# Performance work log

Measured on AMD Instinct MI355X. Metric: run time of the kernel, lower is better.

## Reference

```python
import jax, jax.numpy as jnp
import numpy as np

INFLUENCE_RADIUS = 8  # VectorizedTrajectoryComputer default


def compute_trajectories(emb):
    # emb: [B, S, D] -> [B, S, D]
    B, S, D = emb.shape
    diffs = emb[:, 1:] - emb[:, :-1]                      # [B, S-1, D]
    mag = jnp.linalg.norm(diffs, axis=-1, keepdims=True)  # [B, S-1, 1]
    ntraj = diffs / jnp.maximum(mag, 1e-8)                # normalized trajectories
    mw = jnp.tanh(mag[..., 0])                            # magnitude weights [B, S-1]
    pos = jnp.arange(S)[:, None]                          # [S, 1]
    j = jnp.arange(S - 1)[None, :]                        # [1, S-1]
    ws = jnp.maximum(0, pos - INFLUENCE_RADIUS)           # window start per pos
    mask = (j >= ws) & (j < pos)                          # window_end = pos (pos <= S-1)
    wsz = jnp.maximum(pos - ws, 1)                        # window size (>=1 to avoid /0)
    recency = jnp.where(mask, (j - ws + 1) / wsz, 0.0).astype(emb.dtype)  # [S, S-1]
    cw = mw[:, None, :] * recency[None]                   # combined weights [B, S, S-1]
    nw = cw / jnp.maximum(cw.sum(-1, keepdims=True), 1e-8)
    return jnp.einsum('bpj,bjd->bpd', nw, ntraj)          # [B, S, D]


def setup_inputs() -> dict:
    key = jax.random.key(0)
    ks = jax.random.split(key, 6)
    B, S, D = 2, 2048, 1024
    H, K, hd = 16, 16, 64
    return {
        'x': jax.random.normal(ks[0], (B, S, D), dtype=jnp.float32),
        'qkv_w': jax.random.normal(ks[1], (3 * D, D), dtype=jnp.float32) * 0.02,
        'out_w': jax.random.normal(ks[2], (D, D), dtype=jnp.float32) * 0.02,
        'splat_centers': jax.random.normal(ks[3], (H, K, hd), dtype=jnp.float32) * 0.02,
        'splat_log_scales': jnp.zeros((H, K), dtype=jnp.float32),
        'splat_amplitudes': jnp.ones((H, K), dtype=jnp.float32),
    }


def reference(x, qkv_w, out_w, splat_centers, splat_log_scales, splat_amplitudes):
    B, S, D = x.shape
    H, K, hd = splat_centers.shape
    # trajectories (computed when trajectories=None in forward)
    traj = compute_trajectories(x)
    # qkv projection (no bias)
    qkv = x @ qkv_w.T                                      # [B, S, 3D]
    q, k, v = jnp.split(qkv, 3, axis=-1)
    def heads(t):
        return t.reshape(B, S, H, hd).transpose(0, 2, 1, 3)  # [B, H, S, hd]
    q, k, v = heads(q), heads(k), heads(v)
    # squared distances to splat centers: [B, H, S, K]
    cn = jnp.sum(splat_centers ** 2, axis=-1)              # [H, K]
    def dists_sq(t):
        tn = jnp.sum(t ** 2, axis=-1, keepdims=True)       # [B, H, S, 1]
        cross = jnp.einsum('bhsd,hkd->bhsk', t, splat_centers)
        return tn - 2.0 * cross + cn[None, :, None, :]
    scales_sq = jnp.exp(splat_log_scales)[None, :, None, :] ** 2  # [1, H, 1, K]
    amp = jax.nn.sigmoid(splat_amplitudes)[None, :, None, :]
    q_weights = jnp.exp(-0.5 * dists_sq(q) / scales_sq) * amp     # [B, H, S, K]
    k_weights = jnp.exp(-0.5 * dists_sq(k) / scales_sq) * amp
    attn = jnp.einsum('bhis,bhjs->bhij', q_weights, k_weights)    # [B, H, S, S]
    attn = jax.nn.softmax(attn, axis=-1)
    out = jnp.einsum('bhij,bhjd->bhid', attn, v)                  # [B, H, S, hd]
    out = out.transpose(0, 2, 1, 3).reshape(B, S, D) @ out_w.T    # [B, S, D]
    return out, traj
```

## Files before the change

### kernel.cpp

```cpp
#include <hip/hip_runtime.h>
#include <math.h>

#define SEQ 2048
#define DIM 1024
#define NB  2
#define NH  16

typedef __attribute__((ext_vector_type(8))) short short8;
typedef __attribute__((ext_vector_type(4))) float floatx4;
typedef __attribute__((ext_vector_type(16))) float floatx16;

__device__ __forceinline__ ushort f2bf(float f) {
    unsigned u = __float_as_uint(f);
    return (ushort)((u + 0x7FFFu + ((u >> 16) & 1u)) >> 16);
}
__device__ __forceinline__ float bf2f(ushort h) {
    return __uint_as_float(((unsigned)h) << 16);
}
__device__ __forceinline__ void gload16(const void* g, char* lds_base) {
    __builtin_amdgcn_global_load_lds(
        (const __attribute__((address_space(1))) void*)g,
        (__attribute__((address_space(3))) void*)lds_base, 16, 0, 0);
}
__device__ __forceinline__ unsigned cvtpk(float a, float b) {
    unsigned r;
    asm("v_cvt_pk_bf16_f32 %0, %1, %2" : "=v"(r) : "v"(a), "v"(b));
    return r;
}
__device__ __forceinline__ void plswap(unsigned &a, unsigned &b) {
    asm("v_permlane32_swap_b32 %0, %1" : "+v"(a), "+v"(b));
}

__global__ __launch_bounds__(256) void cvt_split_kernel(
    const float* __restrict__ src, ushort* __restrict__ hi, ushort* __restrict__ lo, int n)
{
    int i = (blockIdx.x * 256 + threadIdx.x) * 4;
    if (i >= n) return;
    float4 v = *(const float4*)(src + i);
    ushort4 h, l;
    h.x = f2bf(v.x); l.x = f2bf(v.x - bf2f(h.x));
    h.y = f2bf(v.y); l.y = f2bf(v.y - bf2f(h.y));
    h.z = f2bf(v.z); l.z = f2bf(v.z - bf2f(h.z));
    h.w = f2bf(v.w); l.w = f2bf(v.w - bf2f(h.w));
    *(ushort4*)(hi + i) = h;
    *(ushort4*)(lo + i) = l;
}

__global__ __launch_bounds__(256) void cvt_front_kernel(
    const float* __restrict__ x, const float* __restrict__ qkv_w,
    ushort* __restrict__ xh, ushort* __restrict__ xl,
    ushort* __restrict__ wh, ushort* __restrict__ wlv)
{
    const int blk = blockIdx.x;
    if (blk < 4096) {
        int i = blk * 1024 + threadIdx.x * 4;
        float4 v = *(const float4*)(x + i);
        ushort4 h, l;
        h.x = f2bf(v.x); l.x = f2bf(v.x - bf2f(h.x));
        h.y = f2bf(v.y); l.y = f2bf(v.y - bf2f(h.y));
        h.z = f2bf(v.z); l.z = f2bf(v.z - bf2f(h.z));
        h.w = f2bf(v.w); l.w = f2bf(v.w - bf2f(h.w));
        *(ushort4*)(xh + i) = h;
        *(ushort4*)(xl + i) = l;
    } else if (blk < 6144) {
        int i = (blk - 4096) * 1024 + threadIdx.x * 4;
        float4 v = *(const float4*)(qkv_w + i);
        ushort4 o;
        o.x = f2bf(v.x); o.y = f2bf(v.y); o.z = f2bf(v.z); o.w = f2bf(v.w);
        *(ushort4*)(wh + i) = o;
    } else {
        int i = (blk - 6144) * 1024 + threadIdx.x * 4;
        float4 v = *(const float4*)(qkv_w + 2097152 + i);
        ushort4 h, l;
        h.x = f2bf(v.x); l.x = f2bf(v.x - bf2f(h.x));
        h.y = f2bf(v.y); l.y = f2bf(v.y - bf2f(h.y));
        h.z = f2bf(v.z); l.z = f2bf(v.z - bf2f(h.z));
        h.w = f2bf(v.w); l.w = f2bf(v.w - bf2f(h.w));
        *(ushort4*)(wh + 2097152 + i) = h;
        *(ushort4*)(wlv + i) = l;
    }
}

__global__ __launch_bounds__(256) void traj_stats_kernel(
    const float* __restrict__ x, float* __restrict__ sbuf, float* __restrict__ invbuf)
{
    const int wave = threadIdx.x >> 6;
    const int lane = threadIdx.x & 63;
    const int row  = blockIdx.x * 4 + wave;
    const int NR = NB * (SEQ - 1);
    if (row >= NR) return;
    const int b = row / (SEQ - 1);
    const int j = row - b * (SEQ - 1);
    const float* x0 = x + ((size_t)(b * SEQ + j)) * DIM;
    const float* x1 = x0 + DIM;
    float sum = 0.f;
    #pragma unroll
    for (int q = 0; q < 4; ++q) {
        int idx = q * 256 + lane * 4;
        float4 a = *(const float4*)(x0 + idx);
        float4 c = *(const float4*)(x1 + idx);
        float dx = c.x-a.x, dy = c.y-a.y, dz = c.z-a.z, dw = c.w-a.w;
        sum += dx*dx + dy*dy + dz*dz + dw*dw;
    }
    #pragma unroll
    for (int off = 32; off > 0; off >>= 1) sum += __shfl_down(sum, off);
    if (lane == 0) {
        float mag = sqrtf(sum);
        sbuf[row]   = tanhf(mag);
        invbuf[row] = 1.0f / fmaxf(mag, 1e-8f);
    }
}

__global__ __launch_bounds__(256) void traj_kernel(
    const float* __restrict__ x, const float* __restrict__ sbuf,
    const float* __restrict__ invbuf, float* __restrict__ traj_out)
{
    const int bp = blockIdx.x;
    const int b  = bp >> 11;
    const int p  = bp & (SEQ - 1);
    int ws = p - 8; if (ws < 0) ws = 0;
    const int wlen = p - ws;
    const float wsz = (float)((p - ws) > 1 ? (p - ws) : 1);
    const int base = b * (SEQ - 1) + ws;

    float Z = 0.f;
    for (int t = 0; t < wlen; ++t)
        Z += sbuf[base + t] * ((float)(t + 1) / wsz);
    const float scale = 1.0f / fmaxf(Z, 1e-8f);

    const int d0 = threadIdx.x * 4;
    const float* xb = x + ((size_t)(b * SEQ + ws)) * DIM + d0;
    float4 prev = *(const float4*)xb;
    float4 acc = make_float4(0.f,0.f,0.f,0.f);
    for (int t = 0; t < wlen; ++t) {
        xb += DIM;
        float4 cur = *(const float4*)xb;
        float cc = sbuf[base + t] * ((float)(t + 1) / wsz) * invbuf[base + t] * scale;
        acc.x += cc * (cur.x - prev.x);
        acc.y += cc * (cur.y - prev.y);
        acc.z += cc * (cur.z - prev.z);
        acc.w += cc * (cur.w - prev.w);
        prev = cur;
    }
    *(float4*)(traj_out + (size_t)bp * DIM + d0) = acc;
}

template<int SPLIT, int EPI, int BN>
__global__ __launch_bounds__(256) void mfma_gemm(
    const ushort* __restrict__ Ah, const ushort* __restrict__ Al,
    const ushort* __restrict__ Bh, const ushort* __restrict__ Bl,
    float* __restrict__ cout, int ldc,
    ushort* __restrict__ qwb, ushort* __restrict__ kwb)
{
    constexpr int JT   = BN / 32;
    constexpr int BSZ  = BN * 64;
    constexpr int HALF = 8192 + BSZ;
    constexpr int SMEM = (SPLIT ? 2 : 1) * HALF;
    __shared__ __align__(16) char smem[SMEM];
    const int tid = threadIdx.x;
    const int l = tid & 63;
    const int w = tid >> 6;
    const int wm = w >> 1, wn = w & 1;
    const int n0 = blockIdx.x * BN;
    const int m0 = blockIdx.y * 128;

    char* a_h = smem;
    char* b_h = smem + 8192;
    char* a_l = smem + HALF;
    char* b_l = smem + HALF + 8192;

    const int srowA = 32 * w + (l >> 2);
    const int srowB = (BN == 128 ? 32 * w : 16 * w) + (l >> 2);
    const int scol  = (l & 3) * 8;
    const ushort* Ahg = Ah + (size_t)(m0 + srowA) * 1024 + scol;
    const ushort* Bhg = Bh + (size_t)(n0 + srowB) * 1024 + scol;
    const ushort* Alg = SPLIT ? Al + (size_t)(m0 + srowA) * 1024 + scol : nullptr;
    const ushort* Blg = SPLIT ? Bl + (size_t)(n0 + srowB) * 1024 + scol : nullptr;

    floatx4 acc[4][JT] = {};
    const int fr = l & 15;
    const int fq = (l >> 4) * 16;

    for (int kb = 0; kb < 1024; kb += 32) {
        if (kb) __syncthreads();
        gload16(Ahg + kb,             a_h + w*2048);
        gload16(Ahg + kb + 16*1024,   a_h + w*2048 + 1024);
        if (BN == 128) {
            gload16(Bhg + kb,             b_h + w*2048);
            gload16(Bhg + kb + 16*1024,   b_h + w*2048 + 1024);
        } else {
            gload16(Bhg + kb,             b_h + w*1024);
        }
        if (SPLIT) {
            gload16(Alg + kb,           a_l + w*2048);
            gload16(Alg + kb + 16*1024, a_l + w*2048 + 1024);
            if (BN == 128) {
                gload16(Blg + kb,           b_l + w*2048);
                gload16(Blg + kb + 16*1024, b_l + w*2048 + 1024);
            } else {
                gload16(Blg + kb,           b_l + w*1024);
            }
        }
        __syncthreads();
        short8 fah[4], fbh[JT], fal[4], fbl[JT];
        #pragma unroll
        for (int t = 0; t < 4; ++t) {
            fah[t] = *(const short8*)(a_h + ((wm*64 + t*16 + fr) << 6) + fq);
            if (SPLIT)
                fal[t] = *(const short8*)(a_l + ((wm*64 + t*16 + fr) << 6) + fq);
        }
        #pragma unroll
        for (int t = 0; t < JT; ++t) {
            fbh[t] = *(const short8*)(b_h + ((wn*(BN/2) + t*16 + fr) << 6) + fq);
            if (SPLIT)
                fbl[t] = *(const short8*)(b_l + ((wn*(BN/2) + t*16 + fr) << 6) + fq);
        }
        #pragma unroll
        for (int it = 0; it < 4; ++it)
            #pragma unroll
            for (int jt = 0; jt < JT; ++jt) {
                acc[it][jt] = __builtin_amdgcn_mfma_f32_16x16x32_bf16(
                    fah[it], fbh[jt], acc[it][jt], 0, 0, 0);
                if (SPLIT) {
                    acc[it][jt] = __builtin_amdgcn_mfma_f32_16x16x32_bf16(
                        fah[it], fbl[jt], acc[it][jt], 0, 0, 0);
                    acc[it][jt] = __builtin_amdgcn_mfma_f32_16x16x32_bf16(
                        fal[it], fbh[jt], acc[it][jt], 0, 0, 0);
                }
            }
    }

    const int row0 = (l >> 4) * 4;
    const int col  = l & 15;

    if (EPI == 0) {
        #pragma unroll
        for (int it = 0; it < 4; ++it)
            #pragma unroll
            for (int jt = 0; jt < JT; ++jt)
                #pragma unroll
                for (int r = 0; r < 4; ++r) {
                    int gm = m0 + wm*64 + it*16 + row0 + r;
                    int gn = n0 + wn*(BN/2) + jt*16 + col;
                    cout[(size_t)gm * ldc + gn] = acc[it][jt][r];
                }
    } else if (EPI == 2) {
        #pragma unroll
        for (int it = 0; it < 4; ++it)
            #pragma unroll
            for (int jt = 0; jt < JT; ++jt)
                #pragma unroll
                for (int r = 0; r < 4; ++r) {
                    int md = m0 + wm*64 + it*16 + row0 + r;
                    int t  = n0 + wn*(BN/2) + jt*16 + col;
                    int bb = t >> 11, ss = t & (SEQ - 1);
                    qwb[((size_t)bb << 21) + (size_t)md * SEQ + ss] = f2bf(acc[it][jt][r]);
                }
    } else {
        ushort* obuf = (n0 < 1024) ? qwb : kwb;
        const int nb = n0 & 1023;
        #pragma unroll
        for (int it = 0; it < 4; ++it)
            #pragma unroll
            for (int jt = 0; jt < JT; ++jt)
                #pragma unroll
                for (int r = 0; r < 4; ++r) {
                    int gm = m0 + wm*64 + it*16 + row0 + r;
                    int gn = nb + wn*(BN/2) + jt*16 + col;
                    int hh = gn >> 6, d = gn & 63;
                    int bb = gm >> 11, ss = gm & (SEQ - 1);
                    obuf[(((size_t)(bb*NH + hh))*SEQ + ss)*64 + d] = f2bf(acc[it][jt][r]);
                }
    }
}

__global__ __launch_bounds__(256) void splat_kernel(
    const ushort* __restrict__ qin, const ushort* __restrict__ kin,
    ushort* __restrict__ wq, ushort* __restrict__ wk,
    const float* __restrict__ centers, const float* __restrict__ lscales,
    const float* __restrict__ amps)
{
    __shared__ float Cs[16*64];
    __shared__ float Pr[48];
    const int tid = threadIdx.x;
    const int isK = blockIdx.x >> 8;
    const int bx  = blockIdx.x & 255;
    const ushort* qk = isK ? kin : qin;
    ushort* wout = isK ? wk : wq;
    const int bh  = bx >> 3;
    const int h   = bh & 15;
    const int s   = (bx & 7) * 256 + tid;
    {
        float4 c4 = *(const float4*)(centers + (size_t)h*1024 + tid*4);
        *(float4*)(Cs + tid*4) = c4;
    }
    if (tid < 16) {
        float s2 = __expf(2.f * lscales[h*16 + tid]);
        Pr[tid]      = -0.5f / s2;
        Pr[16 + tid] = 1.f / (1.f + __expf(-amps[h*16 + tid]));
        const float* cp = centers + ((size_t)h*16 + tid)*64;
        float cn = 0.f;
        for (int i = 0; i < 64; ++i) cn += cp[i]*cp[i];
        Pr[32 + tid] = cn;
    }
    __syncthreads();

    float q[64];
    const ushort* qp = qk + ((size_t)bh*SEQ + s)*64;
    #pragma unroll
    for (int i = 0; i < 8; ++i) {
        short8 v = *(const short8*)(qp + i*8);
        #pragma unroll
        for (int j = 0; j < 8; ++j) q[i*8+j] = bf2f((ushort)v[j]);
    }
    float tn = 0.f;
    #pragma unroll
    for (int i = 0; i < 64; ++i) tn = fmaf(q[i], q[i], tn);

    ushort o16[16];
    #pragma unroll 4
    for (int sp = 0; sp < 16; ++sp) {
        const float* cp = Cs + sp*64;
        float cr = 0.f;
        #pragma unroll
        for (int i = 0; i < 64; ++i) cr = fmaf(q[i], cp[i], cr);
        float dq = tn - 2.f*cr + Pr[32 + sp];
        o16[sp] = f2bf(__expf(dq * Pr[sp]) * Pr[16 + sp]);
    }
    ushort* op = wout + ((size_t)bh*SEQ + s)*16;
    *(short8*)(op)     = *(short8*)(o16);
    *(short8*)(op + 8) = *(short8*)(o16 + 8);
}

__global__ __launch_bounds__(256, 4) void attn_kernel(
    const ushort* __restrict__ qw, const ushort* __restrict__ kw,
    const ushort* __restrict__ vbt, ushort* __restrict__ hoh, ushort* __restrict__ hol)
{
    __shared__ __align__(16) char smem[16384 + 512];
    const int tid = threadIdx.x;
    const int l   = tid & 63;
    const int w   = tid >> 6;
    const int qh  = w >> 1;
    const int kh  = w & 1;
    const int l31 = l & 31;
    const int hi  = l >> 5;
    const int bh = blockIdx.y;
    const int b = bh >> 4;
    const int h = bh & 15;
    const int s0 = blockIdx.x * 64;

    short8 qf = *(const short8*)(qw + ((size_t)bh*SEQ + s0 + qh*32 + l31)*16 + hi*8);

    const ushort* kfp = kw + ((size_t)bh*SEQ + kh*32 + l31)*16 + hi*8;
    const ushort* vtb = vbt + ((size_t)(b*1024 + h*64))*SEQ;

    const int dA = w*16 + (l >> 3);
    const int dB = dA + 8;
    const ushort* vsA = vtb + (size_t)dA*SEQ + ((l & 7) ^ (dA & 7))*8;
    const ushort* vsB = vtb + (size_t)dB*SEQ + ((l & 7) ^ (dB & 7))*8;

    floatx16 acc0 = {}, acc1 = {};
    floatx16 zero16 = {};
    float zpart = 0.f;

    gload16(vsA, smem + w*2048);
    gload16(vsB, smem + w*2048 + 1024);
    short8 kf = *(const short8*)kfp;

    for (int jt = 0; jt < 32; ++jt) {
        __syncthreads();
        char* bufn = smem + ((jt + 1) & 1)*8192;
        if (jt < 31) {
            gload16(vsA + (jt + 1)*64, bufn + w*2048);
            gload16(vsB + (jt + 1)*64, bufn + w*2048 + 1024);
        }
        floatx16 sc = __builtin_amdgcn_mfma_f32_32x32x16_bf16(kf, qf, zero16, 0, 0, 0);
        if (jt < 31) kf = *(const short8*)(kfp + (jt + 1)*1024);

        float e[16];
        #pragma unroll
        for (int r = 0; r < 16; ++r) e[r] = __expf(sc[r]);
        float zs = 0.f;
        #pragma unroll
        for (int r = 0; r < 16; ++r) zs += e[r];
        zpart += zs;

        unsigned p0 = cvtpk(e[0],  e[1]),  p1 = cvtpk(e[2],  e[3]);
        unsigned p2 = cvtpk(e[4],  e[5]),  p3 = cvtpk(e[6],  e[7]);
        unsigned p4 = cvtpk(e[8],  e[9]),  p5 = cvtpk(e[10], e[11]);
        unsigned p6 = cvtpk(e[12], e[13]), p7 = cvtpk(e[14], e[15]);
        plswap(p0, p2); plswap(p1, p3);
        plswap(p4, p6); plswap(p5, p7);
        union { unsigned u[4]; short8 s; } ua, ub;
        ua.u[0] = p0; ua.u[1] = p1; ua.u[2] = p2; ua.u[3] = p3;
        ub.u[0] = p4; ub.u[1] = p5; ub.u[2] = p6; ub.u[3] = p7;

        const ushort* buf = (const ushort*)(smem + (jt & 1)*8192);
        #pragma unroll
        for (int dt = 0; dt < 2; ++dt) {
            int row = dt*32 + l31;
            const ushort* vr = buf + row*64;
            int bk0 = (kh*4 + hi)     ^ (row & 7);
            int bk1 = (kh*4 + 2 + hi) ^ (row & 7);
            short8 vb0 = *(const short8*)(vr + bk0*8);
            short8 vb1 = *(const short8*)(vr + bk1*8);
            if (dt == 0) {
                acc0 = __builtin_amdgcn_mfma_f32_32x32x16_bf16(ua.s, vb0, acc0, 0, 0, 0);
                acc0 = __builtin_amdgcn_mfma_f32_32x32x16_bf16(ub.s, vb1, acc0, 0, 0, 0);
            } else {
                acc1 = __builtin_amdgcn_mfma_f32_32x32x16_bf16(ua.s, vb0, acc1, 0, 0, 0);
                acc1 = __builtin_amdgcn_mfma_f32_32x32x16_bf16(ub.s, vb1, acc1, 0, 0, 0);
            }
        }
    }

    __syncthreads();

    float* cb = (float*)smem;
    float* zb = (float*)(smem + 16384);

    unsigned za = __float_as_uint(zpart), zc = za;
    plswap(za, zc);
    float zq = __uint_as_float(za) + __uint_as_float(zc);
    if (l31 == l) zb[kh*64 + qh*32 + l31] = zq;

    if (kh) {
        #pragma unroll
        for (int r = 0; r < 16; ++r) {
            int q = (r & 3) + 8*(r >> 2) + 4*hi;
            cb[(qh*32 + q)*64 + l31]      = acc0[r];
            cb[(qh*32 + q)*64 + 32 + l31] = acc1[r];
        }
    }
    __syncthreads();
    if (!kh) {
        #pragma unroll
        for (int r = 0; r < 16; ++r) {
            int q = (r & 3) + 8*(r >> 2) + 4*hi;
            float zt = zb[qh*32 + q] + zb[64 + qh*32 + q];
            float inv = 1.0f / zt;
            int s = s0 + qh*32 + q;
            size_t base = ((size_t)(b*SEQ + s))*1024 + h*64;
            float v0 = (acc0[r] + cb[(qh*32 + q)*64 + l31])      * inv;
            float v1 = (acc1[r] + cb[(qh*32 + q)*64 + 32 + l31]) * inv;
            ushort h0 = f2bf(v0);
            ushort h1 = f2bf(v1);
            hoh[base + l31]      = h0;
            hol[base + l31]      = f2bf(v0 - bf2f(h0));
            hoh[base + 32 + l31] = h1;
            hol[base + 32 + l31] = f2bf(v1 - bf2f(h1));
        }
    }
}

extern "C" void kernel_launch(void* const* d_in, const int* in_sizes, int n_in,
                              void* d_out, int out_size, void* d_ws, size_t ws_size,
                              hipStream_t stream)
{
    const float* x       = (const float*)d_in[0];
    const float* qkv_w   = (const float*)d_in[1];
    const float* out_w   = (const float*)d_in[2];
    const float* centers = (const float*)d_in[3];
    const float* lscales = (const float*)d_in[4];
    const float* amps    = (const float*)d_in[5];
    float* out  = (float*)d_out;
    float* traj = out + (size_t)NB*SEQ*DIM;

    char* wsb = (char*)d_ws;
    ushort* xh   = (ushort*)(wsb);
    ushort* xl   = (ushort*)(wsb + (8u<<20));
    ushort* wh   = (ushort*)(wsb + (16u<<20));
    ushort* wlv  = (ushort*)(wsb + (22u<<20));
    ushort* vbt  = (ushort*)(wsb + (24u<<20));
    float*  sbuf = (float*)(wsb + (40u<<20));
    float*  invb = sbuf + 4096;
    ushort* qbuf = xl;
    ushort* kbuf = (ushort*)(wsb + (32u<<20));
    ushort* qwbh = wlv;
    ushort* kwbh = wh + 2048*1024;
    ushort* owh  = wh;
    ushort* owl  = wh + 1048576;
    ushort* hoh  = xh;
    ushort* hol  = xl;

    cvt_front_kernel<<<7168, 256, 0, stream>>>(x, qkv_w, xh, xl, wh, wlv);
    traj_stats_kernel<<<1024, 256, 0, stream>>>(x, sbuf, invb);
    traj_kernel<<<NB*SEQ, 256, 0, stream>>>(x, sbuf, invb, traj);
    mfma_gemm<1,2,64><<<dim3(64, 8), 256, 0, stream>>>(
        wh + 2048*1024, wlv, xh, xl, nullptr, 0, vbt, nullptr);
    mfma_gemm<0,3,128><<<dim3(16, 32), 256, 0, stream>>>(
        xh, nullptr, wh, nullptr, nullptr, 0, qbuf, kbuf);
    splat_kernel<<<512, 256, 0, stream>>>(qbuf, kbuf, qwbh, kwbh, centers, lscales, amps);
    cvt_split_kernel<<<1024, 256, 0, stream>>>(out_w, owh, owl, 1048576);
    attn_kernel<<<dim3(32, 32), 256, 0, stream>>>(qwbh, kwbh, vbt, hoh, hol);
    mfma_gemm<1,0,64><<<dim3(16, 32), 256, 0, stream>>>(
        hoh, hol, owh, owl, out, 1024, nullptr, nullptr);
}
```

Measured before the change: 270.5 us.

## Merge independent small kernels into combined launches to cut kernel count

Folds the trajectory-stats pass into the front conversion kernel and the out_w conversion into the splat kernel. It also splits the trajectory kernel across the V and QK GEMM launches via block-index dispatch, taking the launch count from nine to six. The aim is to remove launch overhead and the tail bubbles between small kernels by letting independent work fill idle CUs. In exchange, the GEMM launches carry the larger LDS footprint on the trajectory blocks too, which could lower occupancy for those blocks.

```diff
diff --git a/kernel.cpp b/kernel.cpp
--- a/kernel.cpp
+++ b/kernel.cpp
@@ -31,25 +31,11 @@
     asm("v_permlane32_swap_b32 %0, %1" : "+v"(a), "+v"(b));
 }
 
-__global__ __launch_bounds__(256) void cvt_split_kernel(
-    const float* __restrict__ src, ushort* __restrict__ hi, ushort* __restrict__ lo, int n)
-{
-    int i = (blockIdx.x * 256 + threadIdx.x) * 4;
-    if (i >= n) return;
-    float4 v = *(const float4*)(src + i);
-    ushort4 h, l;
-    h.x = f2bf(v.x); l.x = f2bf(v.x - bf2f(h.x));
-    h.y = f2bf(v.y); l.y = f2bf(v.y - bf2f(h.y));
-    h.z = f2bf(v.z); l.z = f2bf(v.z - bf2f(h.z));
-    h.w = f2bf(v.w); l.w = f2bf(v.w - bf2f(h.w));
-    *(ushort4*)(hi + i) = h;
-    *(ushort4*)(lo + i) = l;
-}
-
-__global__ __launch_bounds__(256) void cvt_front_kernel(
+__global__ __launch_bounds__(256) void front_kernel(
     const float* __restrict__ x, const float* __restrict__ qkv_w,
     ushort* __restrict__ xh, ushort* __restrict__ xl,
-    ushort* __restrict__ wh, ushort* __restrict__ wlv)
+    ushort* __restrict__ wh, ushort* __restrict__ wlv,
+    float* __restrict__ sbuf, float* __restrict__ invbuf)
 {
     const int blk = blockIdx.x;
     if (blk < 4096) {
@@ -68,7 +54,7 @@
         ushort4 o;
         o.x = f2bf(v.x); o.y = f2bf(v.y); o.z = f2bf(v.z); o.w = f2bf(v.w);
         *(ushort4*)(wh + i) = o;
-    } else {
+    } else if (blk < 7168) {
         int i = (blk - 6144) * 1024 + threadIdx.x * 4;
         float4 v = *(const float4*)(qkv_w + 2097152 + i);
         ushort4 h, l;
@@ -78,44 +64,39 @@
         h.w = f2bf(v.w); l.w = f2bf(v.w - bf2f(h.w));
         *(ushort4*)(wh + 2097152 + i) = h;
         *(ushort4*)(wlv + i) = l;
-    }
-}
-
-__global__ __launch_bounds__(256) void traj_stats_kernel(
-    const float* __restrict__ x, float* __restrict__ sbuf, float* __restrict__ invbuf)
-{
-    const int wave = threadIdx.x >> 6;
-    const int lane = threadIdx.x & 63;
-    const int row  = blockIdx.x * 4 + wave;
-    const int NR = NB * (SEQ - 1);
-    if (row >= NR) return;
-    const int b = row / (SEQ - 1);
-    const int j = row - b * (SEQ - 1);
-    const float* x0 = x + ((size_t)(b * SEQ + j)) * DIM;
-    const float* x1 = x0 + DIM;
-    float sum = 0.f;
-    #pragma unroll
-    for (int q = 0; q < 4; ++q) {
-        int idx = q * 256 + lane * 4;
-        float4 a = *(const float4*)(x0 + idx);
-        float4 c = *(const float4*)(x1 + idx);
-        float dx = c.x-a.x, dy = c.y-a.y, dz = c.z-a.z, dw = c.w-a.w;
-        sum += dx*dx + dy*dy + dz*dz + dw*dw;
-    }
-    #pragma unroll
-    for (int off = 32; off > 0; off >>= 1) sum += __shfl_down(sum, off);
-    if (lane == 0) {
-        float mag = sqrtf(sum);
-        sbuf[row]   = tanhf(mag);
-        invbuf[row] = 1.0f / fmaxf(mag, 1e-8f);
-    }
-}
-
-__global__ __launch_bounds__(256) void traj_kernel(
-    const float* __restrict__ x, const float* __restrict__ sbuf,
+    } else {
+        const int wave = threadIdx.x >> 6;
+        const int lane = threadIdx.x & 63;
+        const int row  = (blk - 7168) * 4 + wave;
+        const int NR = NB * (SEQ - 1);
+        if (row >= NR) return;
+        const int b = row / (SEQ - 1);
+        const int j = row - b * (SEQ - 1);
+        const float* x0 = x + ((size_t)(b * SEQ + j)) * DIM;
+        const float* x1 = x0 + DIM;
+        float sum = 0.f;
+        #pragma unroll
+        for (int q = 0; q < 4; ++q) {
+            int idx = q * 256 + lane * 4;
+            float4 a = *(const float4*)(x0 + idx);
+            float4 c = *(const float4*)(x1 + idx);
+            float dx = c.x-a.x, dy = c.y-a.y, dz = c.z-a.z, dw = c.w-a.w;
+            sum += dx*dx + dy*dy + dz*dz + dw*dw;
+        }
+        #pragma unroll
+        for (int off = 32; off > 0; off >>= 1) sum += __shfl_down(sum, off);
+        if (lane == 0) {
+            float mag = sqrtf(sum);
+            sbuf[row]   = tanhf(mag);
+            invbuf[row] = 1.0f / fmaxf(mag, 1e-8f);
+        }
+    }
+}
+
+__device__ __forceinline__ void traj_body(
+    int bp, const float* __restrict__ x, const float* __restrict__ sbuf,
     const float* __restrict__ invbuf, float* __restrict__ traj_out)
 {
-    const int bp = blockIdx.x;
     const int b  = bp >> 11;
     const int p  = bp & (SEQ - 1);
     int ws = p - 8; if (ws < 0) ws = 0;
@@ -146,7 +127,8 @@
 }
 
 template<int SPLIT, int EPI, int BN>
-__global__ __launch_bounds__(256) void mfma_gemm(
+__device__ __forceinline__ void gemm_body(
+    int bx, int by, char* smem,
     const ushort* __restrict__ Ah, const ushort* __restrict__ Al,
     const ushort* __restrict__ Bh, const ushort* __restrict__ Bl,
     float* __restrict__ cout, int ldc,
@@ -155,14 +137,12 @@
     constexpr int JT   = BN / 32;
     constexpr int BSZ  = BN * 64;
     constexpr int HALF = 8192 + BSZ;
-    constexpr int SMEM = (SPLIT ? 2 : 1) * HALF;
-    __shared__ __align__(16) char smem[SMEM];
     const int tid = threadIdx.x;
     const int l = tid & 63;
     const int w = tid >> 6;
     const int wm = w >> 1, wn = w & 1;
-    const int n0 = blockIdx.x * BN;
-    const int m0 = blockIdx.y * 128;
+    const int n0 = bx * BN;
+    const int m0 = by * 128;
 
     char* a_h = smem;
     char* b_h = smem + 8192;
@@ -274,15 +254,71 @@
     }
 }
 
-__global__ __launch_bounds__(256) void splat_kernel(
+__global__ __launch_bounds__(256) void gemmV_traj_kernel(
+    const ushort* __restrict__ Ah, const ushort* __restrict__ Al,
+    const ushort* __restrict__ Bh, const ushort* __restrict__ Bl,
+    ushort* __restrict__ vbt,
+    const float* __restrict__ x, const float* __restrict__ sbuf,
+    const float* __restrict__ invbuf, float* __restrict__ traj_out)
+{
+    __shared__ __align__(16) char smem[2 * (8192 + 64*64)];
+    const int blk = blockIdx.x;
+    if (blk < 512) {
+        gemm_body<1,2,64>(blk & 63, blk >> 6, smem, Ah, Al, Bh, Bl,
+                          nullptr, 0, vbt, nullptr);
+    } else {
+        traj_body(blk - 512, x, sbuf, invbuf, traj_out);
+    }
+}
+
+__global__ __launch_bounds__(256) void gemmQK_traj_kernel(
+    const ushort* __restrict__ Ah, const ushort* __restrict__ Bh,
+    ushort* __restrict__ qbuf, ushort* __restrict__ kbuf,
+    const float* __restrict__ x, const float* __restrict__ sbuf,
+    const float* __restrict__ invbuf, float* __restrict__ traj_out)
+{
+    __shared__ __align__(16) char smem[8192 + 128*64];
+    const int blk = blockIdx.x;
+    if (blk < 512) {
+        gemm_body<0,3,128>(blk & 15, blk >> 4, smem, Ah, nullptr, Bh, nullptr,
+                           nullptr, 0, qbuf, kbuf);
+    } else {
+        traj_body(blk - 512 + 2048, x, sbuf, invbuf, traj_out);
+    }
+}
+
+__global__ __launch_bounds__(256) void gemmO_kernel(
+    const ushort* __restrict__ Ah, const ushort* __restrict__ Al,
+    const ushort* __restrict__ Bh, const ushort* __restrict__ Bl,
+    float* __restrict__ cout)
+{
+    __shared__ __align__(16) char smem[2 * (8192 + 64*64)];
+    gemm_body<1,0,64>(blockIdx.x, blockIdx.y, smem, Ah, Al, Bh, Bl,
+                      cout, 1024, nullptr, nullptr);
+}
+
+__global__ __launch_bounds__(256) void splat_cvt_kernel(
     const ushort* __restrict__ qin, const ushort* __restrict__ kin,
     ushort* __restrict__ wq, ushort* __restrict__ wk,
     const float* __restrict__ centers, const float* __restrict__ lscales,
-    const float* __restrict__ amps)
+    const float* __restrict__ amps,
+    const float* __restrict__ out_w, ushort* __restrict__ owh, ushort* __restrict__ owl)
 {
     __shared__ float Cs[16*64];
     __shared__ float Pr[48];
     const int tid = threadIdx.x;
+    if (blockIdx.x >= 512) {
+        int i = (blockIdx.x - 512) * 1024 + tid * 4;
+        float4 v = *(const float4*)(out_w + i);
+        ushort4 h, l;
+        h.x = f2bf(v.x); l.x = f2bf(v.x - bf2f(h.x));
+        h.y = f2bf(v.y); l.y = f2bf(v.y - bf2f(h.y));
+        h.z = f2bf(v.z); l.z = f2bf(v.z - bf2f(h.z));
+        h.w = f2bf(v.w); l.w = f2bf(v.w - bf2f(h.w));
+        *(ushort4*)(owh + i) = h;
+        *(ushort4*)(owl + i) = l;
+        return;
+    }
     const int isK = blockIdx.x >> 8;
     const int bx  = blockIdx.x & 255;
     const ushort* qk = isK ? kin : qin;
@@ -483,16 +519,13 @@
     ushort* hoh  = xh;
     ushort* hol  = xl;
 
-    cvt_front_kernel<<<7168, 256, 0, stream>>>(x, qkv_w, xh, xl, wh, wlv);
-    traj_stats_kernel<<<1024, 256, 0, stream>>>(x, sbuf, invb);
-    traj_kernel<<<NB*SEQ, 256, 0, stream>>>(x, sbuf, invb, traj);
-    mfma_gemm<1,2,64><<<dim3(64, 8), 256, 0, stream>>>(
-        wh + 2048*1024, wlv, xh, xl, nullptr, 0, vbt, nullptr);
-    mfma_gemm<0,3,128><<<dim3(16, 32), 256, 0, stream>>>(
-        xh, nullptr, wh, nullptr, nullptr, 0, qbuf, kbuf);
-    splat_kernel<<<512, 256, 0, stream>>>(qbuf, kbuf, qwbh, kwbh, centers, lscales, amps);
-    cvt_split_kernel<<<1024, 256, 0, stream>>>(out_w, owh, owl, 1048576);
+    front_kernel<<<8192, 256, 0, stream>>>(x, qkv_w, xh, xl, wh, wlv, sbuf, invb);
+    gemmV_traj_kernel<<<2560, 256, 0, stream>>>(
+        wh + 2048*1024, wlv, xh, xl, vbt, x, sbuf, invb, traj);
+    gemmQK_traj_kernel<<<2560, 256, 0, stream>>>(
+        xh, wh, qbuf, kbuf, x, sbuf, invb, traj);
+    splat_cvt_kernel<<<1536, 256, 0, stream>>>(
+        qbuf, kbuf, qwbh, kwbh, centers, lscales, amps, out_w, owh, owl);
     attn_kernel<<<dim3(32, 32), 256, 0, stream>>>(qwbh, kwbh, vbt, hoh, hol);
-    mfma_gemm<1,0,64><<<dim3(16, 32), 256, 0, stream>>>(
-        hoh, hol, owh, owl, out, 1024, nullptr, nullptr);
-}
+    gemmO_kernel<<<dim3(16, 32), 256, 0, stream>>>(hoh, hol, owh, owl, out);
+}
```

New measurement: 245.8 us. 1.1x faster.
